# Optimization experiments

Measured on AMD Instinct MI355X. Metric: run time of the kernel, lower is better.

## Reference

```python
import jax, jax.numpy as jnp
import numpy as np

N = 50000      # nodes
E = 800000     # edges (avg degree 16)
D = 128        # in_dim
H = 128        # hidden_dim
C = 10         # n_classes
G = 128        # graphs in batch
N_HID = 3      # hidden_layers (total convs = 1 + N_HID)


def setup_inputs() -> dict:
    key = jax.random.key(0)
    ks = jax.random.split(key, 10)
    s = 0.05  # weight init scale
    x = jax.random.normal(ks[0], (N, D), jnp.float32)
    edge_index = jax.random.randint(ks[1], (2, E), 0, N, dtype=jnp.int32)
    graph_ids = jnp.sort(jax.random.randint(ks[2], (N,), 0, G, dtype=jnp.int32))
    W0 = jax.random.normal(ks[3], (D, H), jnp.float32) * s
    b0 = jnp.zeros((H,), jnp.float32)
    Ws = jax.random.normal(ks[4], (N_HID, H, H), jnp.float32) * s
    bs = jnp.zeros((N_HID, H), jnp.float32)
    Wc = jax.random.normal(ks[5], (H, C), jnp.float32) * s
    bc = jnp.zeros((C,), jnp.float32)
    return {"x": x, "W0": W0, "b0": b0, "Ws": Ws, "bs": bs,
            "Wc": Wc, "bc": bc, "edge_index": edge_index, "graph_ids": graph_ids}


def reference(x, W0, b0, Ws, bs, Wc, bc, edge_index, graph_ids):
    src, dst = edge_index[0], edge_index[1]
    ones_e = jnp.ones((E,), x.dtype)
    # DGL GraphConv norm='both': D_out^{-1/2} on source side, D_in^{-1/2} on dest side
    out_deg = jax.ops.segment_sum(ones_e, src, num_segments=N)
    in_deg = jax.ops.segment_sum(ones_e, dst, num_segments=N)
    c_src = jnp.clip(out_deg, 1.0) ** -0.5  # [N]
    c_dst = jnp.clip(in_deg, 1.0) ** -0.5   # [N]

    def conv(h, W, b):
        # h' = relu( c_dst * A (c_src * h) W + b ); dropout is identity in eval mode
        h = h * c_src[:, None]
        m = jax.ops.segment_sum(h[src], dst, num_segments=N)  # gather + scatter-add
        m = m * c_dst[:, None]
        return jax.nn.relu(m @ W + b)

    h = conv(x, W0, b0)
    for i in range(N_HID):  # fixed small layer count
        h = conv(h, Ws[i], bs[i])

    # mean readout per graph
    cnt = jax.ops.segment_sum(jnp.ones((N,), h.dtype), graph_ids, num_segments=G)
    hg = jax.ops.segment_sum(h, graph_ids, num_segments=G) / jnp.clip(cnt, 1.0)[:, None]
    return hg @ Wc + bc  # [G, C]
```

## Files before the change

kernel.cpp:

```cpp
#include <hip/hip_runtime.h>

#define N_NODES 50000
#define N_EDGES 800000
#define DIM     128
#define NGRAPH  128
#define NCLASS  10
#define NLAYER  4

#define TEAMS   256
#define ESLICE  (N_EDGES / TEAMS)
#define CWORDS  12500
#define DUMMY   50000
#define PRE_BLOCKS 12501

typedef __attribute__((ext_vector_type(8))) short short8;
typedef __attribute__((ext_vector_type(4))) float floatx4;

__device__ __forceinline__ unsigned f2bf(float f) {
    union { float f; unsigned u; } v; v.f = f;
    return (v.u + 0x7fffu + ((v.u >> 16) & 1u)) >> 16;
}
__device__ __forceinline__ float bf_lo(unsigned u) { return __uint_as_float(u << 16); }
__device__ __forceinline__ float bf_hi(unsigned u) { return __uint_as_float(u & 0xffff0000u); }

__global__ __launch_bounds__(1024) void count_kernel(
    const int* __restrict__ ei, unsigned* __restrict__ cntw,
    unsigned* __restrict__ colc_fill)
{
    __shared__ unsigned h[CWORDS];
    int team = blockIdx.x, tid = threadIdx.x;
    for (int i = tid; i < CWORDS; i += 1024) h[i] = 0;
    __syncthreads();
    const int e0 = team * ESLICE;
    const int* __restrict__ srcp = ei;
    const int* __restrict__ dstp = ei + N_EDGES;
    for (int e = e0 + tid; e < e0 + ESLICE; e += 1024) {
        int s = srcp[e], d = dstp[e];
        atomicAdd(&h[d >> 2], 1u  << (8 * (d & 3)));
        atomicAdd(&h[s >> 2], 16u << (8 * (s & 3)));
    }
    __syncthreads();
    for (int i = tid; i < CWORDS; i += 1024)
        cntw[(size_t)team * CWORDS + i] = h[i];
    for (int i = blockIdx.x * 1024 + tid; i < N_NODES * 32; i += TEAMS * 1024)
        colc_fill[i] = 0xC350C350u;
}

__global__ __launch_bounds__(1024) void offsets_kernel(
    const unsigned* __restrict__ cntw, unsigned* __restrict__ offsw,
    unsigned* __restrict__ cnt_dense, float* __restrict__ c_src,
    float* __restrict__ c_dst)
{
    __shared__ unsigned ldsC[128 * 64];
    __shared__ unsigned ldsO[128 * 64];
    __shared__ unsigned totG[4 * 256];
    __shared__ unsigned baseW[4 * 64];
    int tid = threadIdx.x;
    int g = tid >> 8;
    int n = tid & 255;
    int n0 = blockIdx.x * 256;
    int w0 = n0 >> 2;
    unsigned carryIn = 0, carryOut = 0;
    for (int ph = 0; ph < 2; ++ph) {
        int t0 = ph * 128;
        for (int i = tid; i < 128 * 64; i += 1024) {
            int tl = i >> 6, wl = i & 63;
            int gw = w0 + wl;
            ldsC[i] = (gw < CWORDS) ? cntw[(size_t)(t0 + tl) * CWORDS + gw] : 0u;
        }
        __syncthreads();
        unsigned locIn = 0, locOut = 0;
        {
            unsigned char* ob = (unsigned char*)ldsO;
            for (int tl = g * 32; tl < g * 32 + 32; ++tl) {
                unsigned wvd = ldsC[tl * 64 + (n >> 2)];
                unsigned b = (wvd >> (8 * (n & 3))) & 255u;
                ob[tl * 256 + n] = (unsigned char)locIn;
                locIn  += (b & 15u);
                locOut += (b >> 4);
            }
        }
        totG[g * 256 + n] = locIn | (locOut << 16);
        __syncthreads();
        unsigned baseIn = 0, sumIn = 0, sumOut = 0;
#pragma unroll
        for (int gg = 0; gg < 4; ++gg) {
            unsigned t = totG[gg * 256 + n];
            if (gg < g) baseIn += (t & 0xffffu);
            sumIn += (t & 0xffffu); sumOut += (t >> 16);
        }
        ((unsigned char*)baseW)[g * 256 + n] = (unsigned char)(carryIn + baseIn);
        carryIn += sumIn; carryOut += sumOut;
        __syncthreads();
        for (int i = tid; i < 128 * 64; i += 1024) {
            int tl = i >> 6, wl = i & 63;
            int gw = w0 + wl;
            if (gw < CWORDS)
                offsw[(size_t)(t0 + tl) * CWORDS + gw] =
                    ldsO[i] + baseW[(tl >> 5) * 64 + wl];
        }
        __syncthreads();
    }
    if (tid < 256) {
        int nn = n0 + tid;
        if (nn < N_NODES) {
            unsigned id_ = carryIn, od = carryOut;
            cnt_dense[nn] = id_ > 64u ? 64u : id_;
            if (id_ < 1u) id_ = 1u;
            if (od < 1u) od = 1u;
            c_dst[nn] = 1.0f / sqrtf((float)id_);
            c_src[nn] = 1.0f / sqrtf((float)od);
        }
    }
}

__global__ __launch_bounds__(1024) void scatter_kernel(
    const int* __restrict__ ei, const unsigned* __restrict__ offsw,
    unsigned short* __restrict__ colc)
{
    __shared__ unsigned h[CWORDS];
    int team = blockIdx.x, tid = threadIdx.x;
    for (int i = tid; i < CWORDS; i += 1024) h[i] = 0;
    __syncthreads();
    const unsigned char* __restrict__ ob =
        (const unsigned char*)offsw + (size_t)team * 50000;
    const int e0 = team * ESLICE;
    const int* __restrict__ srcp = ei;
    const int* __restrict__ dstp = ei + N_EDGES;
    for (int e = e0 + tid; e < e0 + ESLICE; e += 1024) {
        int s = srcp[e], d = dstp[e];
        unsigned old = atomicAdd(&h[d >> 2], 1u << (8 * (d & 3)));
        unsigned pos = (old >> (8 * (d & 3))) & 15u;
        unsigned slot = (unsigned)ob[d] + pos;
        if (slot < 64u) colc[(size_t)d * 64 + slot] = (unsigned short)s;
    }
}

__global__ __launch_bounds__(256) void prep_kernel(
    const float2* __restrict__ x, const float* __restrict__ c_src,
    unsigned* __restrict__ hsA, unsigned* __restrict__ hsB,
    const float* __restrict__ W0, const float* __restrict__ Ws,
    uint4* __restrict__ Wf)
{
    int bid = blockIdx.x;
    if (bid < PRE_BLOCKS) {
        int i = bid * 256 + threadIdx.x;
        if (i >= (N_NODES + 1) * 64) return;
        int row = i >> 6;
        if (row < N_NODES) {
            float c = c_src[row];
            float2 v = x[i];
            hsA[i] = f2bf(v.x * c) | (f2bf(v.y * c) << 16);
        } else {
            hsA[i] = 0u;
            hsB[i] = 0u;
        }
        return;
    }
    int t = (bid - PRE_BLOCKS) * 256 + threadIdx.x;
    if (t >= NLAYER * 2048) return;
    int layer = t >> 11;
    int rem = t & 2047;
    int lane = rem & 63;
    int s = (rem >> 6) & 3;
    int c = rem >> 8;
    int quad = lane >> 4, colw = c * 16 + (lane & 15);
    int k0 = s * 32 + quad * 8;
    const float* W = (layer == 0) ? W0 : Ws + (size_t)(layer - 1) * DIM * DIM;
    uint4 p;
    unsigned* pp = (unsigned*)&p;
#pragma unroll
    for (int j = 0; j < 4; ++j) {
        unsigned lo = f2bf(W[(size_t)(k0 + 2 * j) * DIM + colw]);
        unsigned hi = f2bf(W[(size_t)(k0 + 2 * j + 1) * DIM + colw]);
        pp[j] = lo | (hi << 16);
    }
    Wf[t] = p;
}

__global__ __launch_bounds__(256) void layer_kernel(
    const unsigned* __restrict__ hs, const unsigned short* __restrict__ colc,
    const unsigned* __restrict__ cnt_dense, const uint4* __restrict__ Wf,
    const float* __restrict__ bias, const float* __restrict__ c_dst,
    const float* __restrict__ c_src, unsigned short* __restrict__ out_bf,
    float* __restrict__ out_f32, int last)
{
    __shared__ unsigned Ash[16 * 64];
    char* Ab = (char*)Ash;
    int tid = threadIdx.x;
    int lane = tid & 63;
    int wv = __builtin_amdgcn_readfirstlane(tid >> 6);
    int r0 = blockIdx.x * 16;
    int nb = r0 + wv * 4;
    const unsigned* __restrict__ cw = (const unsigned*)colc;
    const char* __restrict__ hb = (const char*)hs;
    unsigned loff = (unsigned)(lane << 2);

#pragma unroll
    for (int i = 0; i < 4; ++i) {
        int n = nb + i;
        unsigned deg = cnt_dense[n];
        unsigned rowv = cw[(unsigned)n * 32u + (unsigned)(lane & 31)];
        float f0 = 0.f, f1 = 0.f;
        for (unsigned j = 0; j < deg; j += 8) {
#pragma unroll
            for (int k = 0; k < 4; ++k) {
                unsigned w = (unsigned)__builtin_amdgcn_readlane(
                    (int)rowv, (int)(j >> 1) + k);
                unsigned u0 = *(const unsigned*)(hb + ((w & 0xffffu) << 8) + loff);
                unsigned u1 = *(const unsigned*)(hb + ((w >> 16) << 8) + loff);
                f0 += bf_lo(u0); f1 += bf_hi(u0);
                f0 += bf_lo(u1); f1 += bf_hi(u1);
            }
        }
        int il = wv * 4 + i;
        *(unsigned*)(Ab + il * 256 + ((lane << 2) ^ ((il & 7) << 4))) =
            f2bf(f0) | (f2bf(f1) << 16);
    }
    __syncthreads();

    int quad = lane >> 4, m16 = lane & 15;
    union U { uint4 u; short8 s; };
    U a[4];
#pragma unroll
    for (int s = 0; s < 4; ++s)
        a[s].u = *(const uint4*)(
            Ab + m16 * 256 + ((s * 64 + quad * 16) ^ ((m16 & 7) << 4)));

    floatx4 acc[2];
#pragma unroll
    for (int cc = 0; cc < 2; ++cc) {
        int c = wv * 2 + cc;
        floatx4 ac = {0.f, 0.f, 0.f, 0.f};
#pragma unroll
        for (int s = 0; s < 4; ++s) {
            U b; b.u = Wf[(c * 4 + s) * 64 + lane];
            ac = __builtin_amdgcn_mfma_f32_16x16x32_bf16(a[s].s, b.s, ac, 0, 0, 0);
        }
        acc[cc] = ac;
    }

    float cd[4], cs[4];
#pragma unroll
    for (int r = 0; r < 4; ++r) {
        int row = r0 + quad * 4 + r;
        cd[r] = c_dst[row];
        cs[r] = last ? 1.f : c_src[row];
    }
#pragma unroll
    for (int cc = 0; cc < 2; ++cc) {
        int colg = (wv * 2 + cc) * 16 + m16;
        float b = bias[colg];
#pragma unroll
        for (int r = 0; r < 4; ++r) {
            int row = r0 + quad * 4 + r;
            float v = acc[cc][r] * cd[r] + b;
            v = v > 0.f ? v : 0.f;
            if (last) out_f32[(size_t)row * DIM + colg] = v;
            else      out_bf[(size_t)row * DIM + colg] = (unsigned short)f2bf(v * cs[r]);
        }
    }
}

__global__ __launch_bounds__(128) void readout_kernel(
    const float* __restrict__ h, const int* __restrict__ gid,
    float* __restrict__ hg, float* __restrict__ cntg)
{
    int j  = threadIdx.x;
    int n0 = blockIdx.x * 64;
    float acc = 0.f; int cur = -1; int run = 0;
    for (int i = 0; i < 64; ++i) {
        int n = n0 + i;
        if (n >= N_NODES) break;
        int g = gid[n];
        if (g != cur) {
            if (cur >= 0) {
                atomicAdd(&hg[cur * DIM + j], acc);
                if (j == 0) atomicAdd(&cntg[cur], (float)run);
            }
            cur = g; acc = 0.f; run = 0;
        }
        acc += h[(size_t)n * DIM + j];
        run++;
    }
    if (cur >= 0) {
        atomicAdd(&hg[cur * DIM + j], acc);
        if (j == 0) atomicAdd(&cntg[cur], (float)run);
    }
}

__global__ __launch_bounds__(256) void head_kernel(
    const float* __restrict__ hg, const float* __restrict__ cntg,
    const float* __restrict__ Wc, const float* __restrict__ bc,
    float* __restrict__ out)
{
    int idx = blockIdx.x * blockDim.x + threadIdx.x;
    if (idx >= NGRAPH * NCLASS) return;
    int g = idx / NCLASS, c = idx % NCLASS;
    float inv = 1.0f / fmaxf(cntg[g], 1.0f);
    float s = 0.f;
    for (int j = 0; j < DIM; ++j) s = fmaf(hg[g * DIM + j], Wc[j * NCLASS + c], s);
    out[idx] = s * inv + bc[c];
}

extern "C" void kernel_launch(void* const* d_in, const int* in_sizes, int n_in,
                              void* d_out, int out_size, void* d_ws, size_t ws_size,
                              hipStream_t stream)
{
    const float* x   = (const float*)d_in[0];
    const float* W0  = (const float*)d_in[1];
    const float* b0  = (const float*)d_in[2];
    const float* Ws  = (const float*)d_in[3];
    const float* bs  = (const float*)d_in[4];
    const float* Wc  = (const float*)d_in[5];
    const float* bc  = (const float*)d_in[6];
    const int*   ei  = (const int*)d_in[7];
    const int*   gid = (const int*)d_in[8];
    float* out = (float*)d_out;

    char* ws = (char*)d_ws;
    size_t o = 0;
    auto alloc = [&](size_t bytes) {
        size_t r = o; o = (o + bytes + 255) & ~(size_t)255; return r;
    };
    unsigned* cntw      = (unsigned*)(ws + alloc((size_t)TEAMS * CWORDS * 4));
    unsigned* offsw     = (unsigned*)(ws + alloc((size_t)TEAMS * CWORDS * 4));
    unsigned* cnt_dense = (unsigned*)(ws + alloc((size_t)N_NODES * 4));
    float*    c_src     = (float*)(ws + alloc((size_t)N_NODES * 4));
    float*    c_dst     = (float*)(ws + alloc((size_t)N_NODES * 4));
    unsigned short* colc = (unsigned short*)(ws + alloc((size_t)N_NODES * 64 * 2));
    unsigned* hsA       = (unsigned*)(ws + alloc((size_t)(N_NODES + 1) * 64 * 4));
    unsigned* hsB       = (unsigned*)(ws + alloc((size_t)(N_NODES + 1) * 64 * 4));
    float*    hlast     = (float*)(ws + alloc((size_t)N_NODES * DIM * 4));
    uint4*    Wf        = (uint4*)(ws + alloc((size_t)NLAYER * 2048 * 16));
    float*    hg        = (float*)(ws + alloc((size_t)NGRAPH * DIM * 4));
    float*    cntg      = (float*)(ws + alloc((size_t)NGRAPH * 4));

    hipMemsetAsync(hg,   0, (size_t)NGRAPH * DIM * 4, stream);
    hipMemsetAsync(cntg, 0, (size_t)NGRAPH * 4, stream);

    count_kernel<<<TEAMS, 1024, 0, stream>>>(ei, cntw, (unsigned*)colc);
    offsets_kernel<<<(N_NODES + 255) / 256, 1024, 0, stream>>>(
        cntw, offsw, cnt_dense, c_src, c_dst);
    scatter_kernel<<<TEAMS, 1024, 0, stream>>>(ei, offsw, colc);
    prep_kernel<<<PRE_BLOCKS + (NLAYER * 2048 + 255) / 256, 256, 0, stream>>>(
        (const float2*)x, c_src, hsA, hsB, W0, Ws, Wf);

    const int LAYER_BLOCKS = N_NODES / 16;

    for (int l = 0; l < NLAYER; ++l) {
        const float* b = (l == 0) ? b0 : (bs + (size_t)(l - 1) * DIM);
        int last = (l == NLAYER - 1) ? 1 : 0;
        const unsigned* hin = (l & 1) ? hsB : hsA;
        unsigned* hout      = (l & 1) ? hsA : hsB;
        layer_kernel<<<LAYER_BLOCKS, 256, 0, stream>>>(
            hin, colc, cnt_dense, Wf + (size_t)l * 2048, b, c_dst, c_src,
            (unsigned short*)hout, hlast, last);
    }

    readout_kernel<<<(N_NODES + 63) / 64, 128, 0, stream>>>(hlast, gid, hg, cntg);
    head_kernel<<<(NGRAPH * NCLASS + 255) / 256, 256, 0, stream>>>(hg, cntg, Wc, bc, out);
}
```

Baseline: 284.1 us.

## Make layer kernel persistent with atomic tile queue and register-resident weights

Layer kernel now launches a fixed grid of persistent blocks that pull 16-row tiles from a per-layer atomic counter instead of one block per tile. The weight fragments and bias are loaded into registers once per block rather than per tile. The hg/cntg memsets are folded into prep_kernel and the counters are reset in count_kernel, which removes separate memset launches. The aim is to cut block launch overhead, balance uneven degree work across blocks and reduce repeated weight loads. The cost is an extra atomic and barrier per tile plus higher register pressure under the launch bound.

```diff
diff --git a/kernel.cpp b/kernel.cpp
--- a/kernel.cpp
+++ b/kernel.cpp
@@ -12,6 +12,10 @@
 #define CWORDS  12500
 #define DUMMY   50000
 #define PRE_BLOCKS 12501
+#define WBLK    32
+#define ZBLK    65
+#define NTILES  (N_NODES / 16)
+#define LGRID   1280
 
 typedef __attribute__((ext_vector_type(8))) short short8;
 typedef __attribute__((ext_vector_type(4))) float floatx4;
@@ -25,7 +29,7 @@
 
 __global__ __launch_bounds__(1024) void count_kernel(
     const int* __restrict__ ei, unsigned* __restrict__ cntw,
-    unsigned* __restrict__ colc_fill)
+    unsigned* __restrict__ colc_fill, unsigned* __restrict__ qctr)
 {
     __shared__ unsigned h[CWORDS];
     int team = blockIdx.x, tid = threadIdx.x;
@@ -44,6 +48,7 @@
         cntw[(size_t)team * CWORDS + i] = h[i];
     for (int i = blockIdx.x * 1024 + tid; i < N_NODES * 32; i += TEAMS * 1024)
         colc_fill[i] = 0xC350C350u;
+    if (team == 0 && tid < NLAYER) qctr[tid] = 0u;
 }
 
 __global__ __launch_bounds__(1024) void offsets_kernel(
@@ -140,7 +145,7 @@
     const float2* __restrict__ x, const float* __restrict__ c_src,
     unsigned* __restrict__ hsA, unsigned* __restrict__ hsB,
     const float* __restrict__ W0, const float* __restrict__ Ws,
-    uint4* __restrict__ Wf)
+    uint4* __restrict__ Wf, float* __restrict__ hg, float* __restrict__ cntg)
 {
     int bid = blockIdx.x;
     if (bid < PRE_BLOCKS) {
@@ -157,6 +162,12 @@
         }
         return;
     }
+    if (bid >= PRE_BLOCKS + WBLK) {
+        int idx = (bid - PRE_BLOCKS - WBLK) * 256 + threadIdx.x;
+        if (idx < NGRAPH * DIM) hg[idx] = 0.f;
+        else if (idx < NGRAPH * DIM + NGRAPH) cntg[idx - NGRAPH * DIM] = 0.f;
+        return;
+    }
     int t = (bid - PRE_BLOCKS) * 256 + threadIdx.x;
     if (t >= NLAYER * 2048) return;
     int layer = t >> 11;
@@ -178,87 +189,97 @@
     Wf[t] = p;
 }
 
-__global__ __launch_bounds__(256) void layer_kernel(
+__global__ __launch_bounds__(256, 5) void layer_kernel(
     const unsigned* __restrict__ hs, const unsigned short* __restrict__ colc,
     const unsigned* __restrict__ cnt_dense, const uint4* __restrict__ Wf,
     const float* __restrict__ bias, const float* __restrict__ c_dst,
     const float* __restrict__ c_src, unsigned short* __restrict__ out_bf,
-    float* __restrict__ out_f32, int last)
+    float* __restrict__ out_f32, int last, unsigned* __restrict__ qctr)
 {
     __shared__ unsigned Ash[16 * 64];
+    __shared__ unsigned tile_s;
     char* Ab = (char*)Ash;
     int tid = threadIdx.x;
     int lane = tid & 63;
     int wv = __builtin_amdgcn_readfirstlane(tid >> 6);
-    int r0 = blockIdx.x * 16;
-    int nb = r0 + wv * 4;
     const unsigned* __restrict__ cw = (const unsigned*)colc;
     const char* __restrict__ hb = (const char*)hs;
     unsigned loff = (unsigned)(lane << 2);
-
-#pragma unroll
-    for (int i = 0; i < 4; ++i) {
-        int n = nb + i;
-        unsigned deg = cnt_dense[n];
-        unsigned rowv = cw[(unsigned)n * 32u + (unsigned)(lane & 31)];
-        float f0 = 0.f, f1 = 0.f;
-        for (unsigned j = 0; j < deg; j += 8) {
-#pragma unroll
-            for (int k = 0; k < 4; ++k) {
-                unsigned w = (unsigned)__builtin_amdgcn_readlane(
-                    (int)rowv, (int)(j >> 1) + k);
-                unsigned u0 = *(const unsigned*)(hb + ((w & 0xffffu) << 8) + loff);
-                unsigned u1 = *(const unsigned*)(hb + ((w >> 16) << 8) + loff);
-                f0 += bf_lo(u0); f1 += bf_hi(u0);
-                f0 += bf_lo(u1); f1 += bf_hi(u1);
+    int quad = lane >> 4, m16 = lane & 15;
+
+    union U { uint4 u; short8 s; };
+    U breg[2][4];
+#pragma unroll
+    for (int cc = 0; cc < 2; ++cc)
+#pragma unroll
+        for (int s = 0; s < 4; ++s)
+            breg[cc][s].u = Wf[((wv * 2 + cc) * 4 + s) * 64 + lane];
+    float bv[2];
+#pragma unroll
+    for (int cc = 0; cc < 2; ++cc) bv[cc] = bias[(wv * 2 + cc) * 16 + m16];
+
+    for (;;) {
+        if (tid == 0) tile_s = atomicAdd(qctr, 1u);
+        __syncthreads();
+        unsigned tile = tile_s;
+        if (tile >= (unsigned)NTILES) break;
+        int r0 = (int)tile * 16;
+        int nb = r0 + wv * 4;
+
+#pragma unroll
+        for (int i = 0; i < 4; ++i) {
+            int n = nb + i;
+            unsigned deg = cnt_dense[n];
+            unsigned rowv = cw[(unsigned)n * 32u + (unsigned)(lane & 31)];
+            float f0 = 0.f, f1 = 0.f;
+            for (unsigned j = 0; j < deg; j += 8) {
+#pragma unroll
+                for (int k = 0; k < 4; ++k) {
+                    unsigned w = (unsigned)__builtin_amdgcn_readlane(
+                        (int)rowv, (int)(j >> 1) + k);
+                    unsigned u0 = *(const unsigned*)(hb + ((w & 0xffffu) << 8) + loff);
+                    unsigned u1 = *(const unsigned*)(hb + ((w >> 16) << 8) + loff);
+                    f0 += bf_lo(u0); f1 += bf_hi(u0);
+                    f0 += bf_lo(u1); f1 += bf_hi(u1);
+                }
             }
-        }
-        int il = wv * 4 + i;
-        *(unsigned*)(Ab + il * 256 + ((lane << 2) ^ ((il & 7) << 4))) =
-            f2bf(f0) | (f2bf(f1) << 16);
-    }
-    __syncthreads();
-
-    int quad = lane >> 4, m16 = lane & 15;
-    union U { uint4 u; short8 s; };
-    U a[4];
-#pragma unroll
-    for (int s = 0; s < 4; ++s)
-        a[s].u = *(const uint4*)(
-            Ab + m16 * 256 + ((s * 64 + quad * 16) ^ ((m16 & 7) << 4)));
-
-    floatx4 acc[2];
-#pragma unroll
-    for (int cc = 0; cc < 2; ++cc) {
-        int c = wv * 2 + cc;
-        floatx4 ac = {0.f, 0.f, 0.f, 0.f};
-#pragma unroll
-        for (int s = 0; s < 4; ++s) {
-            U b; b.u = Wf[(c * 4 + s) * 64 + lane];
-            ac = __builtin_amdgcn_mfma_f32_16x16x32_bf16(a[s].s, b.s, ac, 0, 0, 0);
-        }
-        acc[cc] = ac;
-    }
-
-    float cd[4], cs[4];
-#pragma unroll
-    for (int r = 0; r < 4; ++r) {
-        int row = r0 + quad * 4 + r;
-        cd[r] = c_dst[row];
-        cs[r] = last ? 1.f : c_src[row];
-    }
-#pragma unroll
-    for (int cc = 0; cc < 2; ++cc) {
-        int colg = (wv * 2 + cc) * 16 + m16;
-        float b = bias[colg];
-#pragma unroll
-        for (int r = 0; r < 4; ++r) {
-            int row = r0 + quad * 4 + r;
-            float v = acc[cc][r] * cd[r] + b;
-            v = v > 0.f ? v : 0.f;
-            if (last) out_f32[(size_t)row * DIM + colg] = v;
-            else      out_bf[(size_t)row * DIM + colg] = (unsigned short)f2bf(v * cs[r]);
-        }
+            int il = wv * 4 + i;
+            *(unsigned*)(Ab + il * 256 + ((lane << 2) ^ ((il & 7) << 4))) =
+                f2bf(f0) | (f2bf(f1) << 16);
+        }
+        __syncthreads();
+
+        U a[4];
+#pragma unroll
+        for (int s = 0; s < 4; ++s)
+            a[s].u = *(const uint4*)(
+                Ab + m16 * 256 + ((s * 64 + quad * 16) ^ ((m16 & 7) << 4)));
+
+        floatx4 acc[2];
+#pragma unroll
+        for (int cc = 0; cc < 2; ++cc) {
+            floatx4 ac = {0.f, 0.f, 0.f, 0.f};
+#pragma unroll
+            for (int s = 0; s < 4; ++s)
+                ac = __builtin_amdgcn_mfma_f32_16x16x32_bf16(
+                    a[s].s, breg[cc][s].s, ac, 0, 0, 0);
+            acc[cc] = ac;
+        }
+
+#pragma unroll
+        for (int cc = 0; cc < 2; ++cc) {
+            int colg = (wv * 2 + cc) * 16 + m16;
+#pragma unroll
+            for (int r = 0; r < 4; ++r) {
+                int row = r0 + quad * 4 + r;
+                float v = acc[cc][r] * c_dst[row] + bv[cc];
+                v = v > 0.f ? v : 0.f;
+                if (last) out_f32[(size_t)row * DIM + colg] = v;
+                else      out_bf[(size_t)row * DIM + colg] =
+                              (unsigned short)f2bf(v * c_src[row]);
+            }
+        }
+        __syncthreads();
     }
 }
 
@@ -335,27 +356,23 @@
     uint4*    Wf        = (uint4*)(ws + alloc((size_t)NLAYER * 2048 * 16));
     float*    hg        = (float*)(ws + alloc((size_t)NGRAPH * DIM * 4));
     float*    cntg      = (float*)(ws + alloc((size_t)NGRAPH * 4));
-
-    hipMemsetAsync(hg,   0, (size_t)NGRAPH * DIM * 4, stream);
-    hipMemsetAsync(cntg, 0, (size_t)NGRAPH * 4, stream);
-
-    count_kernel<<<TEAMS, 1024, 0, stream>>>(ei, cntw, (unsigned*)colc);
+    unsigned* qctr      = (unsigned*)(ws + alloc((size_t)NLAYER * 4));
+
+    count_kernel<<<TEAMS, 1024, 0, stream>>>(ei, cntw, (unsigned*)colc, qctr);
     offsets_kernel<<<(N_NODES + 255) / 256, 1024, 0, stream>>>(
         cntw, offsw, cnt_dense, c_src, c_dst);
     scatter_kernel<<<TEAMS, 1024, 0, stream>>>(ei, offsw, colc);
-    prep_kernel<<<PRE_BLOCKS + (NLAYER * 2048 + 255) / 256, 256, 0, stream>>>(
-        (const float2*)x, c_src, hsA, hsB, W0, Ws, Wf);
-
-    const int LAYER_BLOCKS = N_NODES / 16;
+    prep_kernel<<<PRE_BLOCKS + WBLK + ZBLK, 256, 0, stream>>>(
+        (const float2*)x, c_src, hsA, hsB, W0, Ws, Wf, hg, cntg);
 
     for (int l = 0; l < NLAYER; ++l) {
         const float* b = (l == 0) ? b0 : (bs + (size_t)(l - 1) * DIM);
         int last = (l == NLAYER - 1) ? 1 : 0;
         const unsigned* hin = (l & 1) ? hsB : hsA;
         unsigned* hout      = (l & 1) ? hsA : hsB;
-        layer_kernel<<<LAYER_BLOCKS, 256, 0, stream>>>(
+        layer_kernel<<<LGRID, 256, 0, stream>>>(
             hin, colc, cnt_dense, Wf + (size_t)l * 2048, b, c_dst, c_src,
-            (unsigned short*)hout, hlast, last);
+            (unsigned short*)hout, hlast, last, qctr + l);
     }
 
     readout_kernel<<<(N_NODES + 63) / 64, 128, 0, stream>>>(hlast, gid, hg, cntg);
```

Result: slower. 412.4 us (+45.1%).

## Interleave four-row neighbor gathers and fuse preprocessing kernels into one launch

Applied to the files above, without the earlier changes.

The aggregation loop now processes four destination rows together up to the maximum degree, issuing eight independent gathers per step to expose more memory-level parallelism. Scatter, feature prep, weight packing and readout buffer zeroing are merged into one kernel launch, replacing two memsets and two launches. The tradeoff is extra gather work on padded slots for lower-degree rows and higher register use.

```diff
diff --git a/kernel.cpp b/kernel.cpp
--- a/kernel.cpp
+++ b/kernel.cpp
@@ -11,7 +11,11 @@
 #define ESLICE  (N_EDGES / TEAMS)
 #define CWORDS  12500
 #define DUMMY   50000
-#define PRE_BLOCKS 12501
+
+#define SCAT_B  256
+#define PRE_B   3126
+#define W_B     8
+#define Z_B     17
 
 typedef __attribute__((ext_vector_type(8))) short short8;
 typedef __attribute__((ext_vector_type(4))) float floatx4;
@@ -114,37 +118,36 @@
     }
 }
 
-__global__ __launch_bounds__(1024) void scatter_kernel(
+__global__ __launch_bounds__(1024) void sp_kernel(
     const int* __restrict__ ei, const unsigned* __restrict__ offsw,
-    unsigned short* __restrict__ colc)
-{
-    __shared__ unsigned h[CWORDS];
-    int team = blockIdx.x, tid = threadIdx.x;
-    for (int i = tid; i < CWORDS; i += 1024) h[i] = 0;
-    __syncthreads();
-    const unsigned char* __restrict__ ob =
-        (const unsigned char*)offsw + (size_t)team * 50000;
-    const int e0 = team * ESLICE;
-    const int* __restrict__ srcp = ei;
-    const int* __restrict__ dstp = ei + N_EDGES;
-    for (int e = e0 + tid; e < e0 + ESLICE; e += 1024) {
-        int s = srcp[e], d = dstp[e];
-        unsigned old = atomicAdd(&h[d >> 2], 1u << (8 * (d & 3)));
-        unsigned pos = (old >> (8 * (d & 3))) & 15u;
-        unsigned slot = (unsigned)ob[d] + pos;
-        if (slot < 64u) colc[(size_t)d * 64 + slot] = (unsigned short)s;
-    }
-}
-
-__global__ __launch_bounds__(256) void prep_kernel(
+    unsigned short* __restrict__ colc,
     const float2* __restrict__ x, const float* __restrict__ c_src,
     unsigned* __restrict__ hsA, unsigned* __restrict__ hsB,
     const float* __restrict__ W0, const float* __restrict__ Ws,
-    uint4* __restrict__ Wf)
-{
-    int bid = blockIdx.x;
-    if (bid < PRE_BLOCKS) {
-        int i = bid * 256 + threadIdx.x;
+    uint4* __restrict__ Wf, float* __restrict__ hg, float* __restrict__ cntg)
+{
+    __shared__ unsigned h[CWORDS];
+    int bid = blockIdx.x, tid = threadIdx.x;
+    if (bid < SCAT_B) {
+        int team = bid;
+        for (int i = tid; i < CWORDS; i += 1024) h[i] = 0;
+        __syncthreads();
+        const unsigned char* __restrict__ ob =
+            (const unsigned char*)offsw + (size_t)team * 50000;
+        const int e0 = team * ESLICE;
+        const int* __restrict__ srcp = ei;
+        const int* __restrict__ dstp = ei + N_EDGES;
+        for (int e = e0 + tid; e < e0 + ESLICE; e += 1024) {
+            int s = srcp[e], d = dstp[e];
+            unsigned old = atomicAdd(&h[d >> 2], 1u << (8 * (d & 3)));
+            unsigned pos = (old >> (8 * (d & 3))) & 15u;
+            unsigned slot = (unsigned)ob[d] + pos;
+            if (slot < 64u) colc[(size_t)d * 64 + slot] = (unsigned short)s;
+        }
+        return;
+    }
+    if (bid < SCAT_B + PRE_B) {
+        int i = (bid - SCAT_B) * 1024 + tid;
         if (i >= (N_NODES + 1) * 64) return;
         int row = i >> 6;
         if (row < N_NODES) {
@@ -157,25 +160,31 @@
         }
         return;
     }
-    int t = (bid - PRE_BLOCKS) * 256 + threadIdx.x;
-    if (t >= NLAYER * 2048) return;
-    int layer = t >> 11;
-    int rem = t & 2047;
-    int lane = rem & 63;
-    int s = (rem >> 6) & 3;
-    int c = rem >> 8;
-    int quad = lane >> 4, colw = c * 16 + (lane & 15);
-    int k0 = s * 32 + quad * 8;
-    const float* W = (layer == 0) ? W0 : Ws + (size_t)(layer - 1) * DIM * DIM;
-    uint4 p;
-    unsigned* pp = (unsigned*)&p;
-#pragma unroll
-    for (int j = 0; j < 4; ++j) {
-        unsigned lo = f2bf(W[(size_t)(k0 + 2 * j) * DIM + colw]);
-        unsigned hi = f2bf(W[(size_t)(k0 + 2 * j + 1) * DIM + colw]);
-        pp[j] = lo | (hi << 16);
-    }
-    Wf[t] = p;
+    if (bid < SCAT_B + PRE_B + W_B) {
+        int t = (bid - SCAT_B - PRE_B) * 1024 + tid;
+        if (t >= NLAYER * 2048) return;
+        int layer = t >> 11;
+        int rem = t & 2047;
+        int lane = rem & 63;
+        int s = (rem >> 6) & 3;
+        int c = rem >> 8;
+        int quad = lane >> 4, colw = c * 16 + (lane & 15);
+        int k0 = s * 32 + quad * 8;
+        const float* W = (layer == 0) ? W0 : Ws + (size_t)(layer - 1) * DIM * DIM;
+        uint4 p;
+        unsigned* pp = (unsigned*)&p;
+#pragma unroll
+        for (int j = 0; j < 4; ++j) {
+            unsigned lo = f2bf(W[(size_t)(k0 + 2 * j) * DIM + colw]);
+            unsigned hi = f2bf(W[(size_t)(k0 + 2 * j + 1) * DIM + colw]);
+            pp[j] = lo | (hi << 16);
+        }
+        Wf[t] = p;
+        return;
+    }
+    int idx = (bid - SCAT_B - PRE_B - W_B) * 1024 + tid;
+    if (idx < NGRAPH * DIM) hg[idx] = 0.f;
+    else if (idx < NGRAPH * DIM + NGRAPH) cntg[idx - NGRAPH * DIM] = 0.f;
 }
 
 __global__ __launch_bounds__(256) void layer_kernel(
@@ -196,26 +205,56 @@
     const char* __restrict__ hb = (const char*)hs;
     unsigned loff = (unsigned)(lane << 2);
 
-#pragma unroll
-    for (int i = 0; i < 4; ++i) {
-        int n = nb + i;
-        unsigned deg = cnt_dense[n];
-        unsigned rowv = cw[(unsigned)n * 32u + (unsigned)(lane & 31)];
-        float f0 = 0.f, f1 = 0.f;
-        for (unsigned j = 0; j < deg; j += 8) {
-#pragma unroll
-            for (int k = 0; k < 4; ++k) {
-                unsigned w = (unsigned)__builtin_amdgcn_readlane(
-                    (int)rowv, (int)(j >> 1) + k);
-                unsigned u0 = *(const unsigned*)(hb + ((w & 0xffffu) << 8) + loff);
-                unsigned u1 = *(const unsigned*)(hb + ((w >> 16) << 8) + loff);
-                f0 += bf_lo(u0); f1 += bf_hi(u0);
-                f0 += bf_lo(u1); f1 += bf_hi(u1);
-            }
-        }
-        int il = wv * 4 + i;
+    unsigned dg0 = cnt_dense[nb + 0], dg1 = cnt_dense[nb + 1];
+    unsigned dg2 = cnt_dense[nb + 2], dg3 = cnt_dense[nb + 3];
+    unsigned m01 = dg0 > dg1 ? dg0 : dg1, m23 = dg2 > dg3 ? dg2 : dg3;
+    unsigned mx = m01 > m23 ? m01 : m23;
+    unsigned row0 = cw[(unsigned)(nb + 0) * 32u + (unsigned)(lane & 31)];
+    unsigned row1 = cw[(unsigned)(nb + 1) * 32u + (unsigned)(lane & 31)];
+    unsigned row2 = cw[(unsigned)(nb + 2) * 32u + (unsigned)(lane & 31)];
+    unsigned row3 = cw[(unsigned)(nb + 3) * 32u + (unsigned)(lane & 31)];
+
+    float f00 = 0.f, f01 = 0.f, f10 = 0.f, f11 = 0.f;
+    float f20 = 0.f, f21 = 0.f, f30 = 0.f, f31 = 0.f;
+    for (unsigned j = 0; j < mx; j += 8) {
+#pragma unroll
+        for (int k = 0; k < 4; ++k) {
+            int sl = (int)(j >> 1) + k;
+            unsigned w0 = (unsigned)__builtin_amdgcn_readlane((int)row0, sl);
+            unsigned w1 = (unsigned)__builtin_amdgcn_readlane((int)row1, sl);
+            unsigned w2 = (unsigned)__builtin_amdgcn_readlane((int)row2, sl);
+            unsigned w3 = (unsigned)__builtin_amdgcn_readlane((int)row3, sl);
+            unsigned u00 = *(const unsigned*)(hb + ((w0 & 0xffffu) << 8) + loff);
+            unsigned u01 = *(const unsigned*)(hb + ((w0 >> 16) << 8) + loff);
+            unsigned u10 = *(const unsigned*)(hb + ((w1 & 0xffffu) << 8) + loff);
+            unsigned u11 = *(const unsigned*)(hb + ((w1 >> 16) << 8) + loff);
+            unsigned u20 = *(const unsigned*)(hb + ((w2 & 0xffffu) << 8) + loff);
+            unsigned u21 = *(const unsigned*)(hb + ((w2 >> 16) << 8) + loff);
+            unsigned u30 = *(const unsigned*)(hb + ((w3 & 0xffffu) << 8) + loff);
+            unsigned u31 = *(const unsigned*)(hb + ((w3 >> 16) << 8) + loff);
+            f00 += bf_lo(u00); f01 += bf_hi(u00);
+            f00 += bf_lo(u01); f01 += bf_hi(u01);
+            f10 += bf_lo(u10); f11 += bf_hi(u10);
+            f10 += bf_lo(u11); f11 += bf_hi(u11);
+            f20 += bf_lo(u20); f21 += bf_hi(u20);
+            f20 += bf_lo(u21); f21 += bf_hi(u21);
+            f30 += bf_lo(u30); f31 += bf_hi(u30);
+            f30 += bf_lo(u31); f31 += bf_hi(u31);
+        }
+    }
+    {
+        int il = wv * 4;
         *(unsigned*)(Ab + il * 256 + ((lane << 2) ^ ((il & 7) << 4))) =
-            f2bf(f0) | (f2bf(f1) << 16);
+            f2bf(f00) | (f2bf(f01) << 16);
+        il++;
+        *(unsigned*)(Ab + il * 256 + ((lane << 2) ^ ((il & 7) << 4))) =
+            f2bf(f10) | (f2bf(f11) << 16);
+        il++;
+        *(unsigned*)(Ab + il * 256 + ((lane << 2) ^ ((il & 7) << 4))) =
+            f2bf(f20) | (f2bf(f21) << 16);
+        il++;
+        *(unsigned*)(Ab + il * 256 + ((lane << 2) ^ ((il & 7) << 4))) =
+            f2bf(f30) | (f2bf(f31) << 16);
     }
     __syncthreads();
 
@@ -336,15 +375,11 @@
     float*    hg        = (float*)(ws + alloc((size_t)NGRAPH * DIM * 4));
     float*    cntg      = (float*)(ws + alloc((size_t)NGRAPH * 4));
 
-    hipMemsetAsync(hg,   0, (size_t)NGRAPH * DIM * 4, stream);
-    hipMemsetAsync(cntg, 0, (size_t)NGRAPH * 4, stream);
-
     count_kernel<<<TEAMS, 1024, 0, stream>>>(ei, cntw, (unsigned*)colc);
     offsets_kernel<<<(N_NODES + 255) / 256, 1024, 0, stream>>>(
         cntw, offsw, cnt_dense, c_src, c_dst);
-    scatter_kernel<<<TEAMS, 1024, 0, stream>>>(ei, offsw, colc);
-    prep_kernel<<<PRE_BLOCKS + (NLAYER * 2048 + 255) / 256, 256, 0, stream>>>(
-        (const float2*)x, c_src, hsA, hsB, W0, Ws, Wf);
+    sp_kernel<<<SCAT_B + PRE_B + W_B + Z_B, 1024, 0, stream>>>(
+        ei, offsw, colc, (const float2*)x, c_src, hsA, hsB, W0, Ws, Wf, hg, cntg);
 
     const int LAYER_BLOCKS = N_NODES / 16;
 
```

New measurement: 266.5 us. -6.2%, faster.
